# Kernel tuning notes

Measured on AMD Instinct MI355X. Metric: run time of the kernel, lower is better.

The kernel has to match this reference:

```python
import jax, jax.numpy as jnp
import numpy as np

B, S, D, H = 2, 2048, 1024, 16
HD = D // H  # head dim = 64

def setup_inputs() -> dict:
    key = jax.random.key(0)
    ks = jax.random.split(key, 3)
    scale = 1.0 / np.sqrt(D)
    return {
        "x": jax.random.normal(ks[0], (B, S, D), jnp.float32),
        "W_attn": jax.random.normal(ks[1], (D, 3 * D), jnp.float32) * scale,
        "b_attn": jnp.zeros((3 * D,), jnp.float32),
        "W_proj": jax.random.normal(ks[2], (D, D), jnp.float32) * scale,
        "b_proj": jnp.zeros((D,), jnp.float32),
    }

def reference(x, W_attn, b_attn, W_proj, b_proj):
    b, s, d = x.shape
    qkv = x @ W_attn + b_attn                      # [B,S,3D]
    q, k, v = jnp.split(qkv, 3, axis=-1)
    # [B,S,D] -> [B,H,S,HD]
    def heads(t):
        return t.reshape(b, s, H, HD).transpose(0, 2, 1, 3)
    q, k, v = heads(q), heads(k), heads(v)
    scores = jnp.einsum('bhqd,bhkd->bhqk', q, k) * (1.0 / np.sqrt(HD))
    causal = jnp.tril(jnp.ones((s, s), dtype=bool))
    scores = jnp.where(causal[None, None], scores, -jnp.inf)
    probs = jax.nn.softmax(scores, axis=-1)
    y = jnp.einsum('bhqk,bhkd->bhqd', probs, v)    # [B,H,S,HD]
    y = y.transpose(0, 2, 1, 3).reshape(b, s, d)
    return y @ W_proj + b_proj
```

## Files before the change

kernel.cpp:

```cpp
#include <hip/hip_runtime.h>

typedef __bf16 bf16;
typedef __bf16 bf16x4 __attribute__((ext_vector_type(4)));
typedef __bf16 bf16x8 __attribute__((ext_vector_type(8)));
typedef float f32x4 __attribute__((ext_vector_type(4)));

#define S_LEN 2048
#define D_DIM 1024
#define N_HEAD 16
#define HEAD_DIM 64
#define M_TOK 4096
#define BH 32

#define EXP2F(x) __builtin_amdgcn_exp2f(x)
#define Q_SCALE 0.18033688f

#define SW(r, c) ((c) ^ (((r) & 3) << 4))
#define SIG(r) (((r) & 0x23) | (((r) & 0x04) << 2) | (((r) & 0x18) >> 1))
#define SIGINV(y) (((y) & 0x23) | (((y) >> 2) & 0x04) | (((y) & 0x0C) << 1))

typedef __attribute__((address_space(3))) void lds_void;
typedef const __attribute__((address_space(1))) void gbl_void;

__device__ __forceinline__ void gl_lds16(const bf16* g, bf16* l) {
  __builtin_amdgcn_global_load_lds((gbl_void*)g, (lds_void*)l, 16, 0, 0);
}

__global__ __launch_bounds__(256) void k_cast(const float* __restrict__ x,
                                              bf16* __restrict__ o, int n) {
  int i = (blockIdx.x * 256 + threadIdx.x) * 4;
  if (i >= n) return;
  float4 v = *(const float4*)(x + i);
  bf16x4 w;
  w[0] = (bf16)v.x; w[1] = (bf16)v.y; w[2] = (bf16)v.z; w[3] = (bf16)v.w;
  *(bf16x4*)(o + i) = w;
}

__global__ __launch_bounds__(256) void k_transpose(const float* __restrict__ W,
                                                   bf16* __restrict__ Wt,
                                                   int K, int N) {
  __shared__ float tile[32][33];
  int nb = blockIdx.x, kb = blockIdx.y;
  int t = threadIdx.x;
  int r = t >> 3, c4 = (t & 7) * 4;
  float4 v = *(const float4*)&W[(kb * 32 + r) * N + nb * 32 + c4];
  tile[r][c4 + 0] = v.x; tile[r][c4 + 1] = v.y;
  tile[r][c4 + 2] = v.z; tile[r][c4 + 3] = v.w;
  __syncthreads();
  bf16x4 o;
  #pragma unroll
  for (int i = 0; i < 4; i++) o[i] = (bf16)tile[c4 + i][r];
  *(bf16x4*)&Wt[(nb * 32 + r) * K + kb * 32 + c4] = o;
}

__global__ __launch_bounds__(256, 2)
void k_gemm_qkv(const bf16* __restrict__ A, const bf16* __restrict__ Bt,
                const float* __restrict__ bias,
                bf16* __restrict__ qk, bf16* __restrict__ vT) {
  __shared__ bf16 As[128 * 32];
  __shared__ bf16 Bs[128 * 32];
  const int K = 1024;
  int bn = blockIdx.x, bm = blockIdx.y;
  int t = threadIdx.x;
  int wave = t >> 6, lane = t & 63, c = lane & 15, quad = lane >> 4;
  int wm = wave & 1, wn = wave >> 1;
  int ldrow = lane >> 2, ldcol = (lane & 3) * 8;

  const bf16* Ag = A + (size_t)(bm * 128) * K;
  const bf16* Bg = Bt + (size_t)(bn * 128) * K;

  f32x4 acc[4][4] = {};

  for (int k0 = 0; k0 < K; k0 += 32) {
    __syncthreads();
    #pragma unroll
    for (int q = 0; q < 2; q++) {
      int r0 = (wave * 2 + q) * 16;
      gl_lds16(&Ag[(size_t)(r0 + ldrow) * K + k0 + ldcol], &As[r0 * 32]);
      gl_lds16(&Bg[(size_t)(r0 + ldrow) * K + k0 + ldcol], &Bs[r0 * 32]);
    }
    __syncthreads();
    bf16x8 af[4];
    #pragma unroll
    for (int mt = 0; mt < 4; mt++)
      af[mt] = *(const bf16x8*)&As[(wm * 64 + mt * 16 + c) * 32 + quad * 8];
    #pragma unroll
    for (int nt = 0; nt < 4; nt++) {
      bf16x8 bfr = *(const bf16x8*)&Bs[(wn * 64 + nt * 16 + c) * 32 + quad * 8];
      #pragma unroll
      for (int mt = 0; mt < 4; mt++)
        acc[mt][nt] = __builtin_amdgcn_mfma_f32_16x16x32_bf16(af[mt], bfr, acc[mt][nt], 0, 0, 0);
    }
  }

  #pragma unroll
  for (int nt = 0; nt < 4; nt++) {
    int n = bn * 128 + wn * 64 + nt * 16 + c;
    int which = n >> 10, nl = n & 1023;
    int h = nl >> 6, hd = nl & 63;
    float bv = bias[n];
    #pragma unroll
    for (int mt = 0; mt < 4; mt++) {
      int m0 = bm * 128 + wm * 64 + mt * 16 + quad * 4;
      int b = m0 >> 11, s0 = m0 & 2047;
      int bh = b * N_HEAD + h;
      if (which == 2) {
        bf16x4 o;
        #pragma unroll
        for (int r = 0; r < 4; r++) o[r] = (bf16)(acc[mt][nt][r] + bv);
        *(bf16x4*)&vT[((size_t)bh * HEAD_DIM + hd) * S_LEN + s0] = o;
      } else if (which == 0) {
        #pragma unroll
        for (int r = 0; r < 4; r++)
          qk[(bh * S_LEN + s0 + r) * HEAD_DIM + hd] = (bf16)((acc[mt][nt][r] + bv) * Q_SCALE);
      } else {
        #pragma unroll
        for (int r = 0; r < 4; r++)
          qk[BH * S_LEN * HEAD_DIM + (bh * S_LEN + s0 + r) * HEAD_DIM + hd] = (bf16)(acc[mt][nt][r] + bv);
      }
    }
  }
}

__global__ __launch_bounds__(512, 4)
void k_attn(const bf16* __restrict__ qk, const bf16* __restrict__ vT,
            bf16* __restrict__ y) {
  __shared__ bf16 Ks[2][128][64];
  __shared__ bf16 Vs[2][64][128];
  int bx = blockIdx.x;
  int bh, p;
  if (bx < 256) { bh = bx & 31; p = bx >> 5; }
  else          { int j = bx - 256; bh = j & 31; p = 15 - (j >> 5); }
  int t = threadIdx.x, w = t >> 6, lane = t & 63, c = lane & 15, quad = lane >> 4;
  const bf16* Qg = qk + (size_t)bh * (S_LEN * HEAD_DIM);
  const bf16* Kg = qk + (size_t)(BH + bh) * (S_LEN * HEAD_DIM);
  const bf16* Vg = vT + (size_t)bh * (HEAD_DIM * S_LEN);
  int b = bh >> 4, h = bh & 15;

  const int NKB2 = p + 1;
  const int dthr = w * 16 + c;

  int jK0 = w * 16 + (lane >> 3);
  int jK1 = jK0 + 8;
  int cK  = ((lane & 7) * 8) ^ ((jK0 & 3) << 4);
  int kRow0 = ((jK0 >> 6) << 6) + SIGINV(jK0 & 63);
  int kRow1 = ((jK1 >> 6) << 6) + SIGINV(jK1 & 63);
  const bf16* kSrc0 = Kg + (size_t)kRow0 * HEAD_DIM + cK;
  const bf16* kSrc1 = Kg + (size_t)kRow1 * HEAD_DIM + cK;
  int jV0 = w * 8 + (lane >> 4);
  int cV  = ((lane & 15) * 8) ^ ((jV0 & 3) << 4);
  const bf16* vSrc0 = Vg + (size_t)jV0 * S_LEN + cV;
  const bf16* vSrc1 = vSrc0 + (size_t)4 * S_LEN;

  gl_lds16(kSrc0, &Ks[0][w * 16][0]);
  gl_lds16(kSrc1, &Ks[0][w * 16 + 8][0]);
  gl_lds16(vSrc0, &Vs[0][w * 8][0]);
  gl_lds16(vSrc1, &Vs[0][w * 8 + 4][0]);

  bf16x8 qf[2];
  f32x4 acc[4] = {};
  float mM = -1e30f, lL = 0.f;
  {
    int qr = p * 128 + w * 16 + c;
    qf[0] = *(const bf16x8*)&Qg[qr * HEAD_DIM + quad * 8];
    qf[1] = *(const bf16x8*)&Qg[qr * HEAD_DIM + 32 + quad * 8];
  }

  for (int kb2 = 0; kb2 < NKB2; kb2++) {
    __syncthreads();
    int cur = kb2 & 1, nxt = cur ^ 1;
    if (kb2 + 1 < NKB2) {
      size_t ko = (size_t)(kb2 + 1) * (128 * HEAD_DIM);
      int    vo = (kb2 + 1) * 128;
      gl_lds16(kSrc0 + ko, &Ks[nxt][w * 16][0]);
      gl_lds16(kSrc1 + ko, &Ks[nxt][w * 16 + 8][0]);
      gl_lds16(vSrc0 + vo, &Vs[nxt][w * 8][0]);
      gl_lds16(vSrc1 + vo, &Vs[nxt][w * 8 + 4][0]);
    }

    f32x4 sc[8];
    __builtin_amdgcn_s_setprio(1);
    #pragma unroll
    for (int kt = 0; kt < 8; kt++) {
      int krr = kt * 16 + c;
      bf16x8 kf0 = *(const bf16x8*)&Ks[cur][krr][SW(krr, quad * 8)];
      bf16x8 kf1 = *(const bf16x8*)&Ks[cur][krr][SW(krr, 32 + quad * 8)];
      f32x4 z = {};
      z = __builtin_amdgcn_mfma_f32_16x16x32_bf16(kf0, qf[0], z, 0, 0, 0);
      z = __builtin_amdgcn_mfma_f32_16x16x32_bf16(kf1, qf[1], z, 0, 0, 0);
      sc[kt] = z;
    }
    __builtin_amdgcn_s_setprio(0);

    if (kb2 == p) {
      #pragma unroll
      for (int kt = 0; kt < 8; kt++) {
        int kbase = ((kt >> 2) << 6) + (((kt >> 1) & 1) << 5) + quad * 8 + ((kt & 1) << 2);
        #pragma unroll
        for (int r = 0; r < 4; r++)
          if (kbase + r > dthr) sc[kt][r] = -1e30f;
      }
    }

    bf16x8 pf[4];
    {
      float tm[8];
      #pragma unroll
      for (int kt = 0; kt < 8; kt++)
        tm[kt] = fmaxf(fmaxf(sc[kt][0], sc[kt][1]), fmaxf(sc[kt][2], sc[kt][3]));
      float mx = fmaxf(fmaxf(fmaxf(tm[0], tm[1]), fmaxf(tm[2], tm[3])),
                       fmaxf(fmaxf(tm[4], tm[5]), fmaxf(tm[6], tm[7])));
      mx = fmaxf(mx, __shfl_xor(mx, 16));
      mx = fmaxf(mx, __shfl_xor(mx, 32));
      float mnew = fmaxf(mM, mx);
      float alpha = EXP2F(mM - mnew);
      mM = mnew;
      lL *= alpha;
      #pragma unroll
      for (int dt = 0; dt < 4; dt++)
        #pragma unroll
        for (int r = 0; r < 4; r++) acc[dt][r] *= alpha;
      float ss[4] = {0.f, 0.f, 0.f, 0.f};
      #pragma unroll
      for (int kt = 0; kt < 8; kt++) {
        float e0 = EXP2F(sc[kt][0] - mM), e1 = EXP2F(sc[kt][1] - mM);
        float e2 = EXP2F(sc[kt][2] - mM), e3 = EXP2F(sc[kt][3] - mM);
        pf[kt >> 1][(kt & 1) * 4 + 0] = (bf16)e0;
        pf[kt >> 1][(kt & 1) * 4 + 1] = (bf16)e1;
        pf[kt >> 1][(kt & 1) * 4 + 2] = (bf16)e2;
        pf[kt >> 1][(kt & 1) * 4 + 3] = (bf16)e3;
        ss[kt & 3] += (e0 + e1) + (e2 + e3);
      }
      float sum = (ss[0] + ss[1]) + (ss[2] + ss[3]);
      sum += __shfl_xor(sum, 16);
      sum += __shfl_xor(sum, 32);
      lL += sum;
    }

    __builtin_amdgcn_s_setprio(1);
    #pragma unroll
    for (int ks = 0; ks < 4; ks++) {
      #pragma unroll
      for (int dt = 0; dt < 4; dt++) {
        int vrow = dt * 16 + c;
        bf16x8 vf = *(const bf16x8*)&Vs[cur][vrow][SW(vrow, ks * 32 + quad * 8)];
        acc[dt] = __builtin_amdgcn_mfma_f32_16x16x32_bf16(vf, pf[ks], acc[dt], 0, 0, 0);
      }
    }
    __builtin_amdgcn_s_setprio(0);
  }

  {
    int q = p * 128 + w * 16 + c;
    float linv = 1.0f / lL;
    #pragma unroll
    for (int dt = 0; dt < 4; dt++) {
      bf16x4 o;
      #pragma unroll
      for (int r = 0; r < 4; r++) o[r] = (bf16)(acc[dt][r] * linv);
      *(bf16x4*)&y[((size_t)(b * S_LEN + q) * N_HEAD + h) * HEAD_DIM + dt * 16 + quad * 4] = o;
    }
  }
}

__global__ __launch_bounds__(256, 2)
void k_gemm_proj(const bf16* __restrict__ A, const bf16* __restrict__ Bt,
                 const float* __restrict__ bias, float* __restrict__ out) {
  __shared__ bf16 As[128 * 32];
  __shared__ bf16 Bs[64 * 32];
  const int K = 1024;
  int bn = blockIdx.x, bm = blockIdx.y;
  int t = threadIdx.x;
  int wave = t >> 6, lane = t & 63, c = lane & 15, quad = lane >> 4;
  int wm = wave & 1, wn = wave >> 1;
  int ldrow = lane >> 2, ldcol = (lane & 3) * 8;

  const bf16* Ag = A + (size_t)(bm * 128) * K;
  const bf16* Bg = Bt + (size_t)(bn * 64) * K;

  f32x4 acc[4][2] = {};

  for (int k0 = 0; k0 < K; k0 += 32) {
    __syncthreads();
    #pragma unroll
    for (int q = 0; q < 2; q++) {
      int r0 = (wave * 2 + q) * 16;
      gl_lds16(&Ag[(size_t)(r0 + ldrow) * K + k0 + ldcol], &As[r0 * 32]);
    }
    gl_lds16(&Bg[(size_t)(wave * 16 + ldrow) * K + k0 + ldcol], &Bs[wave * 16 * 32]);
    __syncthreads();
    bf16x8 af[4];
    #pragma unroll
    for (int mt = 0; mt < 4; mt++)
      af[mt] = *(const bf16x8*)&As[(wm * 64 + mt * 16 + c) * 32 + quad * 8];
    #pragma unroll
    for (int nt = 0; nt < 2; nt++) {
      bf16x8 bfr = *(const bf16x8*)&Bs[(wn * 32 + nt * 16 + c) * 32 + quad * 8];
      #pragma unroll
      for (int mt = 0; mt < 4; mt++)
        acc[mt][nt] = __builtin_amdgcn_mfma_f32_16x16x32_bf16(af[mt], bfr, acc[mt][nt], 0, 0, 0);
    }
  }

  #pragma unroll
  for (int nt = 0; nt < 2; nt++) {
    int n = bn * 64 + wn * 32 + nt * 16 + c;
    float bv = bias[n];
    #pragma unroll
    for (int mt = 0; mt < 4; mt++) {
      #pragma unroll
      for (int r = 0; r < 4; r++) {
        int m = bm * 128 + wm * 64 + mt * 16 + quad * 4 + r;
        out[(size_t)m * D_DIM + n] = acc[mt][nt][r] + bv;
      }
    }
  }
}

extern "C" void kernel_launch(void* const* d_in, const int* in_sizes, int n_in,
                              void* d_out, int out_size, void* d_ws, size_t ws_size,
                              hipStream_t stream) {
  const float* x      = (const float*)d_in[0];
  const float* W_attn = (const float*)d_in[1];
  const float* b_attn = (const float*)d_in[2];
  const float* W_proj = (const float*)d_in[3];
  const float* b_proj = (const float*)d_in[4];
  float* out = (float*)d_out;

  bf16* x_bf = (bf16*)d_ws;
  bf16* wat  = x_bf + 4096 * 1024;
  bf16* wpt  = wat + 3072 * 1024;
  bf16* qk   = wpt + 1024 * 1024;
  bf16* vT   = qk + 8 * 1024 * 1024;
  bf16* y_bf = vT + 4 * 1024 * 1024;

  k_cast<<<4096, 256, 0, stream>>>(x, x_bf, 4096 * 1024);
  k_transpose<<<dim3(3072 / 32, 1024 / 32), 256, 0, stream>>>(W_attn, wat, 1024, 3072);
  k_transpose<<<dim3(1024 / 32, 1024 / 32), 256, 0, stream>>>(W_proj, wpt, 1024, 1024);
  k_gemm_qkv<<<dim3(24, 32), 256, 0, stream>>>(x_bf, wat, b_attn, qk, vT);
  k_attn<<<512, 512, 0, stream>>>(qk, vT, y_bf);
  k_gemm_proj<<<dim3(16, 32), 256, 0, stream>>>(y_bf, wpt, b_proj, out);
}
```

Before: 179.6 us.

## Process two 16-row query tiles per wave in attention kernel, halving block size

The attention kernel now uses 4 waves per block instead of 8, and each wave handles 32 query rows as two 16-row tiles that share the same K and V fragments read from LDS. This halves the LDS reads per MFMA and gives more independent MFMA and exp work per wave for latency hiding. In exchange register pressure roughly doubles (two score sets, two accumulators), the launch bound drops to 256 threads with 2 blocks per CU, and each thread issues twice as many global-to-LDS loads per tile.

```diff
diff --git a/kernel.cpp b/kernel.cpp
--- a/kernel.cpp
+++ b/kernel.cpp
@@ -122,7 +122,7 @@
   }
 }
 
-__global__ __launch_bounds__(512, 4)
+__global__ __launch_bounds__(256, 2)
 void k_attn(const bf16* __restrict__ qk, const bf16* __restrict__ vT,
             bf16* __restrict__ y) {
   __shared__ bf16 Ks[2][128][64];
@@ -138,32 +138,32 @@
   int b = bh >> 4, h = bh & 15;
 
   const int NKB2 = p + 1;
-  const int dthr = w * 16 + c;
-
-  int jK0 = w * 16 + (lane >> 3);
-  int jK1 = jK0 + 8;
-  int cK  = ((lane & 7) * 8) ^ ((jK0 & 3) << 4);
-  int kRow0 = ((jK0 >> 6) << 6) + SIGINV(jK0 & 63);
-  int kRow1 = ((jK1 >> 6) << 6) + SIGINV(jK1 & 63);
-  const bf16* kSrc0 = Kg + (size_t)kRow0 * HEAD_DIM + cK;
-  const bf16* kSrc1 = Kg + (size_t)kRow1 * HEAD_DIM + cK;
-  int jV0 = w * 8 + (lane >> 4);
-  int cV  = ((lane & 15) * 8) ^ ((jV0 & 3) << 4);
-  const bf16* vSrc0 = Vg + (size_t)jV0 * S_LEN + cV;
-  const bf16* vSrc1 = vSrc0 + (size_t)4 * S_LEN;
-
-  gl_lds16(kSrc0, &Ks[0][w * 16][0]);
-  gl_lds16(kSrc1, &Ks[0][w * 16 + 8][0]);
-  gl_lds16(vSrc0, &Vs[0][w * 8][0]);
-  gl_lds16(vSrc1, &Vs[0][w * 8 + 4][0]);
-
-  bf16x8 qf[2];
-  f32x4 acc[4] = {};
-  float mM = -1e30f, lL = 0.f;
+  const int dthrA = w * 32 + c;
+  const int dthrB = dthrA + 16;
+
+  int baseK = w * 8 + (lane >> 3);
+  int cK  = ((lane & 7) * 8) ^ ((baseK & 3) << 4);
+  const bf16* kSrc = Kg + (size_t)SIGINV(baseK) * HEAD_DIM + cK;
+  int baseV = w * 4 + (lane >> 4);
+  int cV  = ((lane & 15) * 8) ^ ((baseV & 3) << 4);
+  const bf16* vSrc = Vg + (size_t)baseV * S_LEN + cV;
+
+  #pragma unroll
+  for (int i = 0; i < 4; i++) {
+    gl_lds16(kSrc + (size_t)(32 * i) * HEAD_DIM, &Ks[0][w * 8 + 32 * i][0]);
+    gl_lds16(vSrc + (size_t)(16 * i) * S_LEN,    &Vs[0][w * 4 + 16 * i][0]);
+  }
+
+  bf16x8 qfA[2], qfB[2];
+  f32x4 accA[4] = {}, accB[4] = {};
+  float mMA = -1e30f, lLA = 0.f, mMB = -1e30f, lLB = 0.f;
   {
-    int qr = p * 128 + w * 16 + c;
-    qf[0] = *(const bf16x8*)&Qg[qr * HEAD_DIM + quad * 8];
-    qf[1] = *(const bf16x8*)&Qg[qr * HEAD_DIM + 32 + quad * 8];
+    int qrA = p * 128 + w * 32 + c;
+    qfA[0] = *(const bf16x8*)&Qg[qrA * HEAD_DIM + quad * 8];
+    qfA[1] = *(const bf16x8*)&Qg[qrA * HEAD_DIM + 32 + quad * 8];
+    int qrB = qrA + 16;
+    qfB[0] = *(const bf16x8*)&Qg[qrB * HEAD_DIM + quad * 8];
+    qfB[1] = *(const bf16x8*)&Qg[qrB * HEAD_DIM + 32 + quad * 8];
   }
 
   for (int kb2 = 0; kb2 < NKB2; kb2++) {
@@ -172,23 +172,28 @@
     if (kb2 + 1 < NKB2) {
       size_t ko = (size_t)(kb2 + 1) * (128 * HEAD_DIM);
       int    vo = (kb2 + 1) * 128;
-      gl_lds16(kSrc0 + ko, &Ks[nxt][w * 16][0]);
-      gl_lds16(kSrc1 + ko, &Ks[nxt][w * 16 + 8][0]);
-      gl_lds16(vSrc0 + vo, &Vs[nxt][w * 8][0]);
-      gl_lds16(vSrc1 + vo, &Vs[nxt][w * 8 + 4][0]);
-    }
-
-    f32x4 sc[8];
+      #pragma unroll
+      for (int i = 0; i < 4; i++) {
+        gl_lds16(kSrc + ko + (size_t)(32 * i) * HEAD_DIM, &Ks[nxt][w * 8 + 32 * i][0]);
+        gl_lds16(vSrc + vo + (size_t)(16 * i) * S_LEN,    &Vs[nxt][w * 4 + 16 * i][0]);
+      }
+    }
+
+    f32x4 scA[8], scB[8];
     __builtin_amdgcn_s_setprio(1);
     #pragma unroll
     for (int kt = 0; kt < 8; kt++) {
       int krr = kt * 16 + c;
       bf16x8 kf0 = *(const bf16x8*)&Ks[cur][krr][SW(krr, quad * 8)];
       bf16x8 kf1 = *(const bf16x8*)&Ks[cur][krr][SW(krr, 32 + quad * 8)];
-      f32x4 z = {};
-      z = __builtin_amdgcn_mfma_f32_16x16x32_bf16(kf0, qf[0], z, 0, 0, 0);
-      z = __builtin_amdgcn_mfma_f32_16x16x32_bf16(kf1, qf[1], z, 0, 0, 0);
-      sc[kt] = z;
+      f32x4 za = {};
+      za = __builtin_amdgcn_mfma_f32_16x16x32_bf16(kf0, qfA[0], za, 0, 0, 0);
+      za = __builtin_amdgcn_mfma_f32_16x16x32_bf16(kf1, qfA[1], za, 0, 0, 0);
+      scA[kt] = za;
+      f32x4 zb = {};
+      zb = __builtin_amdgcn_mfma_f32_16x16x32_bf16(kf0, qfB[0], zb, 0, 0, 0);
+      zb = __builtin_amdgcn_mfma_f32_16x16x32_bf16(kf1, qfB[1], zb, 0, 0, 0);
+      scB[kt] = zb;
     }
     __builtin_amdgcn_s_setprio(0);
 
@@ -197,44 +202,56 @@
       for (int kt = 0; kt < 8; kt++) {
         int kbase = ((kt >> 2) << 6) + (((kt >> 1) & 1) << 5) + quad * 8 + ((kt & 1) << 2);
         #pragma unroll
-        for (int r = 0; r < 4; r++)
-          if (kbase + r > dthr) sc[kt][r] = -1e30f;
-      }
-    }
-
-    bf16x8 pf[4];
+        for (int r = 0; r < 4; r++) {
+          if (kbase + r > dthrA) scA[kt][r] = -1e30f;
+          if (kbase + r > dthrB) scB[kt][r] = -1e30f;
+        }
+      }
+    }
+
+    bf16x8 pfA[4], pfB[4];
     {
-      float tm[8];
-      #pragma unroll
-      for (int kt = 0; kt < 8; kt++)
-        tm[kt] = fmaxf(fmaxf(sc[kt][0], sc[kt][1]), fmaxf(sc[kt][2], sc[kt][3]));
-      float mx = fmaxf(fmaxf(fmaxf(tm[0], tm[1]), fmaxf(tm[2], tm[3])),
-                       fmaxf(fmaxf(tm[4], tm[5]), fmaxf(tm[6], tm[7])));
-      mx = fmaxf(mx, __shfl_xor(mx, 16));
-      mx = fmaxf(mx, __shfl_xor(mx, 32));
-      float mnew = fmaxf(mM, mx);
-      float alpha = EXP2F(mM - mnew);
-      mM = mnew;
-      lL *= alpha;
+      float tmA[8], tmB[8];
+      #pragma unroll
+      for (int kt = 0; kt < 8; kt++) {
+        tmA[kt] = fmaxf(fmaxf(scA[kt][0], scA[kt][1]), fmaxf(scA[kt][2], scA[kt][3]));
+        tmB[kt] = fmaxf(fmaxf(scB[kt][0], scB[kt][1]), fmaxf(scB[kt][2], scB[kt][3]));
+      }
+      float mxA = fmaxf(fmaxf(fmaxf(tmA[0], tmA[1]), fmaxf(tmA[2], tmA[3])),
+                        fmaxf(fmaxf(tmA[4], tmA[5]), fmaxf(tmA[6], tmA[7])));
+      float mxB = fmaxf(fmaxf(fmaxf(tmB[0], tmB[1]), fmaxf(tmB[2], tmB[3])),
+                        fmaxf(fmaxf(tmB[4], tmB[5]), fmaxf(tmB[6], tmB[7])));
+      mxA = fmaxf(mxA, __shfl_xor(mxA, 16));
+      mxB = fmaxf(mxB, __shfl_xor(mxB, 16));
+      mxA = fmaxf(mxA, __shfl_xor(mxA, 32));
+      mxB = fmaxf(mxB, __shfl_xor(mxB, 32));
+      float mnA = fmaxf(mMA, mxA), mnB = fmaxf(mMB, mxB);
+      float alA = EXP2F(mMA - mnA), alB = EXP2F(mMB - mnB);
+      mMA = mnA; mMB = mnB;
+      lLA *= alA; lLB *= alB;
       #pragma unroll
       for (int dt = 0; dt < 4; dt++)
         #pragma unroll
-        for (int r = 0; r < 4; r++) acc[dt][r] *= alpha;
-      float ss[4] = {0.f, 0.f, 0.f, 0.f};
+        for (int r = 0; r < 4; r++) { accA[dt][r] *= alA; accB[dt][r] *= alB; }
+      float ssA[4] = {0.f, 0.f, 0.f, 0.f}, ssB[4] = {0.f, 0.f, 0.f, 0.f};
       #pragma unroll
       for (int kt = 0; kt < 8; kt++) {
-        float e0 = EXP2F(sc[kt][0] - mM), e1 = EXP2F(sc[kt][1] - mM);
-        float e2 = EXP2F(sc[kt][2] - mM), e3 = EXP2F(sc[kt][3] - mM);
-        pf[kt >> 1][(kt & 1) * 4 + 0] = (bf16)e0;
-        pf[kt >> 1][(kt & 1) * 4 + 1] = (bf16)e1;
-        pf[kt >> 1][(kt & 1) * 4 + 2] = (bf16)e2;
-        pf[kt >> 1][(kt & 1) * 4 + 3] = (bf16)e3;
-        ss[kt & 3] += (e0 + e1) + (e2 + e3);
-      }
-      float sum = (ss[0] + ss[1]) + (ss[2] + ss[3]);
-      sum += __shfl_xor(sum, 16);
-      sum += __shfl_xor(sum, 32);
-      lL += sum;
+        #pragma unroll
+        for (int r = 0; r < 4; r++) {
+          float ea = EXP2F(scA[kt][r] - mMA);
+          float eb = EXP2F(scB[kt][r] - mMB);
+          pfA[kt >> 1][(kt & 1) * 4 + r] = (bf16)ea;
+          pfB[kt >> 1][(kt & 1) * 4 + r] = (bf16)eb;
+          ssA[r] += ea; ssB[r] += eb;
+        }
+      }
+      float sA = (ssA[0] + ssA[1]) + (ssA[2] + ssA[3]);
+      float sB = (ssB[0] + ssB[1]) + (ssB[2] + ssB[3]);
+      sA += __shfl_xor(sA, 16);
+      sB += __shfl_xor(sB, 16);
+      sA += __shfl_xor(sA, 32);
+      sB += __shfl_xor(sB, 32);
+      lLA += sA; lLB += sB;
     }
 
     __builtin_amdgcn_s_setprio(1);
@@ -244,21 +261,27 @@
       for (int dt = 0; dt < 4; dt++) {
         int vrow = dt * 16 + c;
         bf16x8 vf = *(const bf16x8*)&Vs[cur][vrow][SW(vrow, ks * 32 + quad * 8)];
-        acc[dt] = __builtin_amdgcn_mfma_f32_16x16x32_bf16(vf, pf[ks], acc[dt], 0, 0, 0);
+        accA[dt] = __builtin_amdgcn_mfma_f32_16x16x32_bf16(vf, pfA[ks], accA[dt], 0, 0, 0);
+        accB[dt] = __builtin_amdgcn_mfma_f32_16x16x32_bf16(vf, pfB[ks], accB[dt], 0, 0, 0);
       }
     }
     __builtin_amdgcn_s_setprio(0);
   }
 
   {
-    int q = p * 128 + w * 16 + c;
-    float linv = 1.0f / lL;
+    int qA = p * 128 + w * 32 + c;
+    int qB = qA + 16;
+    float liA = 1.0f / lLA, liB = 1.0f / lLB;
     #pragma unroll
     for (int dt = 0; dt < 4; dt++) {
-      bf16x4 o;
-      #pragma unroll
-      for (int r = 0; r < 4; r++) o[r] = (bf16)(acc[dt][r] * linv);
-      *(bf16x4*)&y[((size_t)(b * S_LEN + q) * N_HEAD + h) * HEAD_DIM + dt * 16 + quad * 4] = o;
+      bf16x4 oA, oB;
+      #pragma unroll
+      for (int r = 0; r < 4; r++) {
+        oA[r] = (bf16)(accA[dt][r] * liA);
+        oB[r] = (bf16)(accB[dt][r] * liB);
+      }
+      *(bf16x4*)&y[((size_t)(b * S_LEN + qA) * N_HEAD + h) * HEAD_DIM + dt * 16 + quad * 4] = oA;
+      *(bf16x4*)&y[((size_t)(b * S_LEN + qB) * N_HEAD + h) * HEAD_DIM + dt * 16 + quad * 4] = oB;
     }
   }
 }
@@ -338,6 +361,6 @@
   k_transpose<<<dim3(3072 / 32, 1024 / 32), 256, 0, stream>>>(W_attn, wat, 1024, 3072);
   k_transpose<<<dim3(1024 / 32, 1024 / 32), 256, 0, stream>>>(W_proj, wpt, 1024, 1024);
   k_gemm_qkv<<<dim3(24, 32), 256, 0, stream>>>(x_bf, wat, b_attn, qk, vT);
-  k_attn<<<512, 512, 0, stream>>>(qk, vT, y_bf);
+  k_attn<<<512, 256, 0, stream>>>(qk, vT, y_bf);
   k_gemm_proj<<<dim3(16, 32), 256, 0, stream>>>(y_bf, wpt, b_proj, out);
 }
```

New measurement: 181.5 us. About the same (+1.0%).
